# Optimization experiments

Hardware: AMD Instinct MI355X
Metric: run time of the kernel (lower is better)

Reference implementation:

```python
import jax, jax.numpy as jnp
import numpy as np

N, DM, F, G, FG = 4096, 512, 128, 8, 16
DH, DE, ES = 128, 256, 4
E = G * ES
GROUP_TOP_K, EXPERT_TOP_K = 2, 2
TEMP = 1.0
LN_EPS = 1e-5


def _ln(x, g, b):
    m = jnp.mean(x, axis=-1, keepdims=True)
    v = jnp.mean((x - m) ** 2, axis=-1, keepdims=True)
    return (x - m) * jax.lax.rsqrt(v + LN_EPS) * g + b


def _topk_softmax(logits, k):
    # faithful to torch _topk_softmax: softmax over top-k values, zeros elsewhere
    vals, idx = jax.lax.top_k(logits, k)
    w = jax.nn.softmax(vals, axis=-1)
    oh = jax.nn.one_hot(idx, logits.shape[-1], dtype=logits.dtype)  # [..., k, E]
    return jnp.einsum('...ke,...k->...e', oh, w)


def setup_inputs() -> dict:
    key = jax.random.key(0)
    ks = iter(jax.random.split(key, 32))
    n = lambda shape, s=0.02: jax.random.normal(next(ks), shape, dtype=jnp.float32) * s
    d = {
        'hidden': jax.random.normal(next(ks), (N, DM), dtype=jnp.float32),
        'feat': jax.random.normal(next(ks), (N, F), dtype=jnp.float32),
        # pre_ln
        'pre_ln_g': jnp.ones((DM,), jnp.float32), 'pre_ln_b': jnp.zeros((DM,), jnp.float32),
        # router_hidden_encoder: LN(DM) -> Lin(DM,DH) -> GELU -> Lin(DH,DH)
        'rh_ln_g': jnp.ones((DM,), jnp.float32), 'rh_ln_b': jnp.zeros((DM,), jnp.float32),
        'rh_w1': n((DM, DH)), 'rh_b1': jnp.zeros((DH,), jnp.float32),
        'rh_w2': n((DH, DH)), 'rh_b2': jnp.zeros((DH,), jnp.float32),
        # stage_feature_encoder: LN(F) -> Lin(F,DH) -> GELU -> Lin(DH,DH)
        'sf_ln_g': jnp.ones((F,), jnp.float32), 'sf_ln_b': jnp.zeros((F,), jnp.float32),
        'sf_w1': n((F, DH)), 'sf_b1': jnp.zeros((DH,), jnp.float32),
        'sf_w2': n((DH, DH)), 'sf_b2': jnp.zeros((DH,), jnp.float32),
        # group_feature_encoders (stacked over G): LN(FG) -> Lin(FG,DH) -> GELU -> Lin(DH,DH)
        'gf_ln_g': jnp.ones((G, FG), jnp.float32), 'gf_ln_b': jnp.zeros((G, FG), jnp.float32),
        'gf_w1': n((G, FG, DH)), 'gf_b1': jnp.zeros((G, DH), jnp.float32),
        'gf_w2': n((G, DH, DH)), 'gf_b2': jnp.zeros((G, DH), jnp.float32),
        # per_group_scorer (ScalarRouter): Lin(4DH,DH) -> GELU -> Lin(DH,1)
        'pgs_w1': n((4 * DH, DH)), 'pgs_b1': jnp.zeros((DH,), jnp.float32),
        'pgs_w2': n((DH,)), 'pgs_b2': jnp.zeros((), jnp.float32),
        # intra_routers (stacked over G): Lin(4DH,DH) -> GELU -> Lin(DH,ES)
        'ir_w1': n((G, 4 * DH, DH)), 'ir_b1': jnp.zeros((G, DH), jnp.float32),
        'ir_w2': n((G, DH, ES)), 'ir_b2': jnp.zeros((G, ES), jnp.float32),
        # experts (stacked over E = G*ES, group-major): Lin(DM,DE) -> GELU -> Lin(DE,DM)
        'ex_w1': n((E, DM, DE)), 'ex_b1': jnp.zeros((E, DE), jnp.float32),
        'ex_w2': n((E, DE, DM)), 'ex_b2': jnp.zeros((E, DM), jnp.float32),
    }
    return d


def reference(hidden, feat, pre_ln_g, pre_ln_b, rh_ln_g, rh_ln_b, rh_w1, rh_b1, rh_w2, rh_b2,
              sf_ln_g, sf_ln_b, sf_w1, sf_b1, sf_w2, sf_b2,
              gf_ln_g, gf_ln_b, gf_w1, gf_b1, gf_w2, gf_b2,
              pgs_w1, pgs_b1, pgs_w2, pgs_b2,
              ir_w1, ir_b1, ir_w2, ir_b2,
              ex_w1, ex_b1, ex_w2, ex_b2):
    # expert input (pre-LN hidden)
    h_norm = _ln(hidden, pre_ln_g, pre_ln_b)                         # [N, DM]

    # factorized router encoders
    h_enc = jax.nn.gelu(_ln(hidden, rh_ln_g, rh_ln_b) @ rh_w1 + rh_b1) @ rh_w2 + rh_b2   # [N, DH]
    s_enc = jax.nn.gelu(_ln(feat, sf_ln_g, sf_ln_b) @ sf_w1 + sf_b1) @ sf_w2 + sf_b2     # [N, DH]
    gfeat = feat.reshape(N, G, FG)                                    # disjoint contiguous group features
    g_h = jax.nn.gelu(jnp.einsum('ngf,gfh->ngh', _ln(gfeat, gf_ln_g, gf_ln_b), gf_w1) + gf_b1)
    g_enc = jnp.einsum('ngh,ghk->ngk', g_h, gf_w2) + gf_b2            # [N, G, DH]

    hB = jnp.broadcast_to(h_enc[:, None, :], (N, G, DH))
    sB = jnp.broadcast_to(s_enc[:, None, :], (N, G, DH))
    router_in = jnp.concatenate([hB, sB, g_enc, hB * g_enc], axis=-1)  # [N, G, 4DH]

    # per-group scalar scores -> group logits -> top-k scatter softmax
    pg_h = jax.nn.gelu(jnp.einsum('ngi,ih->ngh', router_in, pgs_w1) + pgs_b1)
    group_logits = (jnp.einsum('ngh,h->ng', pg_h, pgs_w2) + pgs_b2) / max(TEMP, 1e-6)    # [N, G]
    group_w = _topk_softmax(group_logits, GROUP_TOP_K)                 # [N, G]

    # intra-group expert routers -> top-k scatter softmax over expert_scale
    ir_h = jax.nn.gelu(jnp.einsum('ngi,gih->ngh', router_in, ir_w1) + ir_b1)
    intra_logits = jnp.einsum('ngh,ghe->nge', ir_h, ir_w2) + ir_b2     # [N, G, ES]
    intra_w = _topk_softmax(intra_logits, EXPERT_TOP_K)                # [N, G, ES]

    comb_w = (group_w[:, :, None] * intra_w).reshape(N, E)             # group-major expert order

    # per-expert GELU MLPs on pre-LN hidden (dense compute, sparse weights)
    eh = jax.nn.gelu(jnp.einsum('nd,edh->neh', h_norm, ex_w1) + ex_b1) # [N, E, DE]
    eo = jnp.einsum('neh,ehd->ned', eh, ex_w2) + ex_b2                 # [N, E, DM]
    out = jnp.einsum('ne,ned->nd', comb_w, eo)                         # [N, DM]
    return out
```

## Files before the change

kernel.cpp:

```cpp
#include <hip/hip_runtime.h>
#include <hip/hip_bf16.h>
#include <math.h>

#define N_TOK 4096
#define DM 512
#define FDIM 128
#define G 8
#define FG 16
#define DH 128
#define DE 256
#define ES 4
#define E_EXP 32
#define LN_EPS 1e-5f
#define BT 32

typedef __attribute__((ext_vector_type(8))) short bf16x8;
typedef __attribute__((ext_vector_type(4))) float f32x4;

#define MFMA16(a, b, c) __builtin_amdgcn_mfma_f32_16x16x32_bf16((a), (b), (c), 0, 0, 0)

__device__ __forceinline__ float gelu_t(float x) {
    const float c = 0.7978845608028654f;
    float x3 = x * x * x;
    return 0.5f * x * (1.0f + tanhf(c * (x + 0.044715f * x3)));
}

__device__ __forceinline__ short f2bf(float f) {
    __hip_bfloat16 h = __float2bfloat16(f);
    return *reinterpret_cast<short*>(&h);
}
__device__ __forceinline__ float bf2f(short s) {
    __hip_bfloat16 h = *reinterpret_cast<__hip_bfloat16*>(&s);
    return __bfloat162float(h);
}
__device__ __forceinline__ void split3(float x, short& h, short& m, short& l) {
    h = f2bf(x);
    float r = x - bf2f(h);
    m = f2bf(r);
    float r2 = r - bf2f(m);
    l = f2bf(r2);
}

__global__ void k_ln_hidden(const float* __restrict__ hidden,
                            const float* __restrict__ pg, const float* __restrict__ pb,
                            const float* __restrict__ rg, const float* __restrict__ rb,
                            __hip_bfloat16* __restrict__ h_normb, float* __restrict__ hL) {
    int n = blockIdx.x;
    int j = threadIdx.x;
    const float* x = hidden + (size_t)n * DM;
    float v0 = x[j], v1 = x[j + 256];
    float s = v0 + v1, q = v0 * v0 + v1 * v1;
#pragma unroll
    for (int o = 32; o; o >>= 1) { s += __shfl_down(s, o); q += __shfl_down(q, o); }
    __shared__ float red[8];
    int w = j >> 6;
    if ((j & 63) == 0) { red[w] = s; red[4 + w] = q; }
    __syncthreads();
    float sum = red[0] + red[1] + red[2] + red[3];
    float sq  = red[4] + red[5] + red[6] + red[7];
    float m = sum * (1.0f / DM);
    float var = sq * (1.0f / DM) - m * m;
    float rs = rsqrtf(var + LN_EPS);
    float t0 = (v0 - m) * rs, t1 = (v1 - m) * rs;
    size_t base = (size_t)n * DM;
    h_normb[base + j]       = __float2bfloat16(t0 * pg[j]       + pb[j]);
    h_normb[base + j + 256] = __float2bfloat16(t1 * pg[j + 256] + pb[j + 256]);
    hL[base + j]           = t0 * rg[j]       + rb[j];
    hL[base + j + 256]     = t1 * rg[j + 256] + rb[j + 256];
}

struct ConvJob { const float* src; short* dh; short* dm; short* dl;
                 int KB, NB, Kreal, plain, blk0; };
struct ConvJobs { ConvJob j[10]; };

__global__ void k_conv_all(ConvJobs J) {
    int b = blockIdx.x;
    int ji = 0;
#pragma unroll
    for (int i = 1; i < 10; i++) if (b >= J.j[i].blk0) ji = i;
    const ConvJob jb = J.j[ji];
    int rel = b - jb.blk0;
    int mat = rel / jb.KB, kb = rel % jb.KB;
    int ncols = jb.NB * 16;
    const float* s = jb.src + (size_t)mat * jb.Kreal * ncols;
    size_t dbase = ((size_t)mat * jb.KB + kb) * jb.NB * 512;
    for (int p = threadIdx.x; p < jb.NB * 64; p += 256) {
        int nb = p >> 6, lane = p & 63;
        int row0 = kb * 32 + ((lane >> 4) << 3);
        int col = nb * 16 + (lane & 15);
        if (jb.plain) {
            union { short sh[8]; uint4 v; } t;
#pragma unroll
            for (int j = 0; j < 8; j++) {
                float x = (row0 + j < jb.Kreal) ? s[(size_t)(row0 + j) * ncols + col] : 0.f;
                t.sh[j] = f2bf(x);
            }
            *(uint4*)&jb.dh[dbase + (size_t)p * 8] = t.v;
        } else {
            union { short sh[8]; uint4 v; } hi, mi, lo;
#pragma unroll
            for (int j = 0; j < 8; j++) {
                float x = (row0 + j < jb.Kreal) ? s[(size_t)(row0 + j) * ncols + col] : 0.f;
                split3(x, hi.sh[j], mi.sh[j], lo.sh[j]);
            }
            *(uint4*)&jb.dh[dbase + (size_t)p * 8] = hi.v;
            *(uint4*)&jb.dm[dbase + (size_t)p * 8] = mi.v;
            *(uint4*)&jb.dl[dbase + (size_t)p * 8] = lo.v;
        }
    }
}

template <int KB_TOT, bool DO_LN>
__device__ __forceinline__ void enc2_body(
        int bx, char* smem,
        const float* __restrict__ X,
        const float* __restrict__ lng, const float* __restrict__ lnb,
        const short* __restrict__ W1h, const short* __restrict__ W1m, const short* __restrict__ W1l,
        const float* __restrict__ B1,
        const short* __restrict__ W2h, const short* __restrict__ W2m, const short* __restrict__ W2l,
        const float* __restrict__ B2,
        float* __restrict__ Y) {
    constexpr int K = KB_TOT * 32;
    const int n0 = bx * 32;
    const int tid = threadIdx.x;
    const int wave = tid >> 6, lane = tid & 63;
    const int quad = lane >> 4, lm = lane & 15;
    const int mt = wave & 1;
    const int ngb = (wave >> 1) * 4;

    short (*Ah)[132] = (short(*)[132])smem;
    short (*Am)[132] = (short(*)[132])(smem + 32 * 132 * 2);
    short (*Al)[132] = (short(*)[132])(smem + 2 * 32 * 132 * 2);

    f32x4 acc[4];
#pragma unroll
    for (int i = 0; i < 4; i++) acc[i] = (f32x4)(0.f);

    if (DO_LN) {
        for (int idx = tid; idx < 1024; idx += 256) {
            int row = idx >> 5, c4 = (idx & 31) * 4;
            float4 v = *(const float4*)&X[(size_t)(n0 + row) * K + c4];
            float s = v.x + v.y + v.z + v.w;
            float q = v.x * v.x + v.y * v.y + v.z * v.z + v.w * v.w;
#pragma unroll
            for (int o = 16; o; o >>= 1) { s += __shfl_xor(s, o); q += __shfl_xor(q, o); }
            float mean = s * (1.0f / 128.0f);
            float var = q * (1.0f / 128.0f) - mean * mean;
            float rs = rsqrtf(var + LN_EPS);
            float xv[4] = {(v.x - mean) * rs * lng[c4 + 0] + lnb[c4 + 0],
                           (v.y - mean) * rs * lng[c4 + 1] + lnb[c4 + 1],
                           (v.z - mean) * rs * lng[c4 + 2] + lnb[c4 + 2],
                           (v.w - mean) * rs * lng[c4 + 3] + lnb[c4 + 3]};
#pragma unroll
            for (int j = 0; j < 4; j++) {
                short h, m, l; split3(xv[j], h, m, l);
                Ah[row][c4 + j] = h; Am[row][c4 + j] = m; Al[row][c4 + j] = l;
            }
        }
        __syncthreads();
#pragma unroll
        for (int kb = 0; kb < KB_TOT; kb++) {
            bf16x8 ah = *(const bf16x8*)&Ah[mt * 16 + lm][kb * 32 + quad * 8];
            bf16x8 am = *(const bf16x8*)&Am[mt * 16 + lm][kb * 32 + quad * 8];
            bf16x8 al = *(const bf16x8*)&Al[mt * 16 + lm][kb * 32 + quad * 8];
#pragma unroll
            for (int nt = 0; nt < 4; nt++) {
                size_t bi = (((size_t)kb * 8 + ngb + nt) * 64 + lane) * 8;
                bf16x8 bh = *(const bf16x8*)&W1h[bi];
                bf16x8 bm = *(const bf16x8*)&W1m[bi];
                bf16x8 bl = *(const bf16x8*)&W1l[bi];
                acc[nt] = MFMA16(al, bh, acc[nt]);
                acc[nt] = MFMA16(am, bm, acc[nt]);
                acc[nt] = MFMA16(ah, bl, acc[nt]);
                acc[nt] = MFMA16(am, bh, acc[nt]);
                acc[nt] = MFMA16(ah, bm, acc[nt]);
                acc[nt] = MFMA16(ah, bh, acc[nt]);
            }
        }
    } else {
        for (int kb = 0; kb < KB_TOT; kb++) {
            const float* xs = X + (size_t)(n0 + mt * 16 + lm) * K + kb * 32 + quad * 8;
            float4 x0 = *(const float4*)xs, x1 = *(const float4*)(xs + 4);
            float xv[8] = {x0.x, x0.y, x0.z, x0.w, x1.x, x1.y, x1.z, x1.w};
            bf16x8 ah, am, al;
#pragma unroll
            for (int j = 0; j < 8; j++) {
                short h, m, l; split3(xv[j], h, m, l);
                ah[j] = h; am[j] = m; al[j] = l;
            }
#pragma unroll
            for (int nt = 0; nt < 4; nt++) {
                size_t bi = (((size_t)kb * 8 + ngb + nt) * 64 + lane) * 8;
                bf16x8 bh = *(const bf16x8*)&W1h[bi];
                bf16x8 bm = *(const bf16x8*)&W1m[bi];
                bf16x8 bl = *(const bf16x8*)&W1l[bi];
                acc[nt] = MFMA16(al, bh, acc[nt]);
                acc[nt] = MFMA16(am, bm, acc[nt]);
                acc[nt] = MFMA16(ah, bl, acc[nt]);
                acc[nt] = MFMA16(am, bh, acc[nt]);
                acc[nt] = MFMA16(ah, bm, acc[nt]);
                acc[nt] = MFMA16(ah, bh, acc[nt]);
            }
        }
    }
    __syncthreads();
#pragma unroll
    for (int nt = 0; nt < 4; nt++) {
        int col = (ngb + nt) * 16 + lm;
        float b1 = B1[col];
#pragma unroll
        for (int r = 0; r < 4; r++) {
            int row = mt * 16 + quad * 4 + r;
            short h, m, l; split3(gelu_t(acc[nt][r] + b1), h, m, l);
            Ah[row][col] = h; Am[row][col] = m; Al[row][col] = l;
        }
    }
    __syncthreads();
    f32x4 acc2[4];
#pragma unroll
    for (int i = 0; i < 4; i++) acc2[i] = (f32x4)(0.f);
#pragma unroll
    for (int kb = 0; kb < 4; kb++) {
        bf16x8 ah = *(const bf16x8*)&Ah[mt * 16 + lm][kb * 32 + quad * 8];
        bf16x8 am = *(const bf16x8*)&Am[mt * 16 + lm][kb * 32 + quad * 8];
        bf16x8 al = *(const bf16x8*)&Al[mt * 16 + lm][kb * 32 + quad * 8];
#pragma unroll
        for (int nt = 0; nt < 4; nt++) {
            size_t bi = (((size_t)kb * 8 + ngb + nt) * 64 + lane) * 8;
            bf16x8 bh = *(const bf16x8*)&W2h[bi];
            bf16x8 bm = *(const bf16x8*)&W2m[bi];
            bf16x8 bl = *(const bf16x8*)&W2l[bi];
            acc2[nt] = MFMA16(al, bh, acc2[nt]);
            acc2[nt] = MFMA16(am, bm, acc2[nt]);
            acc2[nt] = MFMA16(ah, bl, acc2[nt]);
            acc2[nt] = MFMA16(am, bh, acc2[nt]);
            acc2[nt] = MFMA16(ah, bm, acc2[nt]);
            acc2[nt] = MFMA16(ah, bh, acc2[nt]);
        }
    }
#pragma unroll
    for (int nt = 0; nt < 4; nt++) {
        int col = (ngb + nt) * 16 + lm;
        float b2 = B2[col];
#pragma unroll
        for (int r = 0; r < 4; r++) {
            int row = mt * 16 + quad * 4 + r;
            Y[(size_t)(n0 + row) * DH + col] = acc2[nt][r] + b2;
        }
    }
}

__device__ __forceinline__ void genc_one(
        int bx, int g, char* smem,
        const float* __restrict__ feat,
        const float* __restrict__ gln_g, const float* __restrict__ gln_b,
        const short* __restrict__ W1h, const short* __restrict__ W1m, const short* __restrict__ W1l,
        const float* __restrict__ gb1,
        const short* __restrict__ W2h, const short* __restrict__ W2m, const short* __restrict__ W2l,
        const float* __restrict__ gb2,
        float* __restrict__ g_enc) {
    const int n0 = bx * 32;
    const int tid = threadIdx.x;
    const int wave = tid >> 6, lane = tid & 63;
    const int quad = lane >> 4, lm = lane & 15;
    const int mt = wave & 1;
    const int ngb = (wave >> 1) * 4;

    short (*Ah)[132] = (short(*)[132])smem;
    short (*Am)[132] = (short(*)[132])(smem + 8448);
    short (*Al)[132] = (short(*)[132])(smem + 2 * 8448);

    {
        int t = tid >> 3, sub = tid & 7;
        const float* fr = feat + (size_t)(n0 + t) * FDIM + g * FG;
        float xv[FG];
        float mean = 0.f;
#pragma unroll
        for (int i = 0; i < FG; i++) { xv[i] = fr[i]; mean += xv[i]; }
        mean *= (1.0f / FG);
        float var = 0.f;
#pragma unroll
        for (int i = 0; i < FG; i++) { float d = xv[i] - mean; var += d * d; }
        var *= (1.0f / FG);
        float rs = rsqrtf(var + LN_EPS);
#pragma unroll
        for (int j = 0; j < 2; j++) {
            int i = sub * 2 + j;
            float xn = (xv[i] - mean) * rs * gln_g[g * FG + i] + gln_b[g * FG + i];
            short h, m, l; split3(xn, h, m, l);
            Ah[t][i] = h; Am[t][i] = m; Al[t][i] = l;
            Ah[t][16 + i] = 0; Am[t][16 + i] = 0; Al[t][16 + i] = 0;
        }
    }
    __syncthreads();
    f32x4 acc[4];
#pragma unroll
    for (int i = 0; i < 4; i++) acc[i] = (f32x4)(0.f);
    {
        bf16x8 ah = *(const bf16x8*)&Ah[mt * 16 + lm][quad * 8];
        bf16x8 am = *(const bf16x8*)&Am[mt * 16 + lm][quad * 8];
        bf16x8 al = *(const bf16x8*)&Al[mt * 16 + lm][quad * 8];
#pragma unroll
        for (int nt = 0; nt < 4; nt++) {
            size_t bi = (((size_t)g * 8 + ngb + nt) * 64 + lane) * 8;
            bf16x8 bh = *(const bf16x8*)&W1h[bi];
            bf16x8 bm = *(const bf16x8*)&W1m[bi];
            bf16x8 bl = *(const bf16x8*)&W1l[bi];
            acc[nt] = MFMA16(al, bh, acc[nt]);
            acc[nt] = MFMA16(am, bm, acc[nt]);
            acc[nt] = MFMA16(ah, bl, acc[nt]);
            acc[nt] = MFMA16(am, bh, acc[nt]);
            acc[nt] = MFMA16(ah, bm, acc[nt]);
            acc[nt] = MFMA16(ah, bh, acc[nt]);
        }
    }
    __syncthreads();
#pragma unroll
    for (int nt = 0; nt < 4; nt++) {
        int col = (ngb + nt) * 16 + lm;
        float b1 = gb1[g * DH + col];
#pragma unroll
        for (int r = 0; r < 4; r++) {
            int row = mt * 16 + quad * 4 + r;
            short h, m, l; split3(gelu_t(acc[nt][r] + b1), h, m, l);
            Ah[row][col] = h; Am[row][col] = m; Al[row][col] = l;
        }
    }
    __syncthreads();
    f32x4 acc2[4];
#pragma unroll
    for (int i = 0; i < 4; i++) acc2[i] = (f32x4)(0.f);
#pragma unroll
    for (int kb = 0; kb < 4; kb++) {
        bf16x8 a2h = *(const bf16x8*)&Ah[mt * 16 + lm][kb * 32 + quad * 8];
        bf16x8 a2m = *(const bf16x8*)&Am[mt * 16 + lm][kb * 32 + quad * 8];
        bf16x8 a2l = *(const bf16x8*)&Al[mt * 16 + lm][kb * 32 + quad * 8];
#pragma unroll
        for (int nt = 0; nt < 4; nt++) {
            size_t bi = ((((size_t)g * 4 + kb) * 8 + ngb + nt) * 64 + lane) * 8;
            bf16x8 bh = *(const bf16x8*)&W2h[bi];
            bf16x8 bm = *(const bf16x8*)&W2m[bi];
            bf16x8 bl = *(const bf16x8*)&W2l[bi];
            acc2[nt] = MFMA16(a2l, bh, acc2[nt]);
            acc2[nt] = MFMA16(a2m, bm, acc2[nt]);
            acc2[nt] = MFMA16(a2h, bl, acc2[nt]);
            acc2[nt] = MFMA16(a2m, bh, acc2[nt]);
            acc2[nt] = MFMA16(a2h, bm, acc2[nt]);
            acc2[nt] = MFMA16(a2h, bh, acc2[nt]);
        }
    }
#pragma unroll
    for (int nt = 0; nt < 4; nt++) {
        int col = (ngb + nt) * 16 + lm;
        float b2 = gb2[g * DH + col];
#pragma unroll
        for (int r = 0; r < 4; r++) {
            int row = mt * 16 + quad * 4 + r;
            g_enc[((size_t)(n0 + row) * G + g) * DH + col] = acc2[nt][r] + b2;
        }
    }
}

__global__ __launch_bounds__(256) void k_enc_all(
        const float* __restrict__ hL, const float* __restrict__ feat,
        const float* __restrict__ sf_g, const float* __restrict__ sf_b,
        const float* __restrict__ gln_g, const float* __restrict__ gln_b,
        const short* Brh1H, const short* Brh1M, const short* Brh1L, const float* rh_b1,
        const short* Brh2H, const short* Brh2M, const short* Brh2L, const float* rh_b2,
        const short* Bsf1H, const short* Bsf1M, const short* Bsf1L, const float* sf_b1,
        const short* Bsf2H, const short* Bsf2M, const short* Bsf2L, const float* sf_b2,
        const short* Bgf1H, const short* Bgf1M, const short* Bgf1L, const float* gf_b1,
        const short* Bgf2H, const short* Bgf2M, const short* Bgf2L, const float* gf_b2,
        float* __restrict__ h_enc, float* __restrict__ s_enc, float* __restrict__ g_enc) {
    __shared__ __align__(16) char smem[3 * 8448];
    int bid = blockIdx.x;
    if (bid < 128)
        enc2_body<16, false>(bid, smem, hL, nullptr, nullptr,
                             Brh1H, Brh1M, Brh1L, rh_b1, Brh2H, Brh2M, Brh2L, rh_b2, h_enc);
    else if (bid < 256)
        enc2_body<4, true>(bid - 128, smem, feat, sf_g, sf_b,
                           Bsf1H, Bsf1M, Bsf1L, sf_b1, Bsf2H, Bsf2M, Bsf2L, sf_b2, s_enc);
    else {
        int idx = bid - 256;
        genc_one(idx >> 3, idx & 7, smem, feat, gln_g, gln_b,
                 Bgf1H, Bgf1M, Bgf1L, gf_b1, Bgf2H, Bgf2M, Bgf2L, gf_b2, g_enc);
    }
}

__global__ void k_stage_hs(const float* __restrict__ h_enc, const float* __restrict__ s_enc,
                           short* __restrict__ Ah, short* __restrict__ Am, short* __restrict__ Al) {
    int T16 = blockIdx.x;
    for (int slot = threadIdx.x; slot < 512; slot += 256) {
        int kb = slot >> 6, lane = slot & 63;
        int quad = lane >> 4, lm = lane & 15;
        int n = T16 * 16 + lm;
        int c0 = kb * 32 + quad * 8;
        const float* src = (c0 < 128) ? (h_enc + (size_t)n * DH + c0)
                                      : (s_enc + (size_t)n * DH + (c0 - 128));
        float4 x0 = *(const float4*)src;
        float4 x1 = *(const float4*)(src + 4);
        float xv[8] = {x0.x, x0.y, x0.z, x0.w, x1.x, x1.y, x1.z, x1.w};
        union { short sh[8]; uint4 v; } hi, mi, lo;
#pragma unroll
        for (int j = 0; j < 8; j++) split3(xv[j], hi.sh[j], mi.sh[j], lo.sh[j]);
        size_t base = ((size_t)T16 * 512 + slot) * 8;
        *(uint4*)&Ah[base] = hi.v;
        *(uint4*)&Am[base] = mi.v;
        *(uint4*)&Al[base] = lo.v;
    }
}

__global__ __launch_bounds__(256) void k_router_mfma(
        const short* __restrict__ AhsH, const short* __restrict__ AhsM, const short* __restrict__ AhsL,
        const float* __restrict__ h_enc, const float* __restrict__ g_enc,
        const short* __restrict__ BpgH, const short* __restrict__ BpgM, const short* __restrict__ BpgL,
        const short* __restrict__ BirH, const short* __restrict__ BirM, const short* __restrict__ BirL,
        const float* __restrict__ pb1, const float* __restrict__ pw2, const float* __restrict__ pb2,
        const float* __restrict__ ib1, const float* __restrict__ iw2, const float* __restrict__ ib2,
        float* __restrict__ glog, float* __restrict__ ilog) {
    const int g = blockIdx.x & 7;
    const int bx = blockIdx.x >> 3;
    const int tid = threadIdx.x;
    const int wave = tid >> 6, lane = tid & 63;
    const int quad = lane >> 4, lm = lane & 15;
    const bool is_pg = wave < 2;
    const int nbase = (wave & 1) * 4;
    const short* Bh = is_pg ? BpgH : (BirH + (size_t)g * 65536);
    const short* Bm = is_pg ? BpgM : (BirM + (size_t)g * 65536);
    const short* Bl = is_pg ? BpgL : (BirL + (size_t)g * 65536);
    const int n0 = bx * 32;

    __shared__ float ph[32][129];
    __shared__ float ih[32][129];

    f32x4 acc[2][4];
#pragma unroll
    for (int mt = 0; mt < 2; mt++)
#pragma unroll
        for (int nt = 0; nt < 4; nt++) acc[mt][nt] = (f32x4)(0.f);

    for (int kb = 0; kb < 16; kb++) {
        bf16x8 Ahf[2], Amf[2], Alf[2];
#pragma unroll
        for (int mt = 0; mt < 2; mt++) {
            if (kb < 8) {
                size_t ai = (((size_t)(2 * bx + mt) * 8 + kb) * 64 + lane) * 8;
                Ahf[mt] = *(const bf16x8*)&AhsH[ai];
                Amf[mt] = *(const bf16x8*)&AhsM[ai];
                Alf[mt] = *(const bf16x8*)&AhsL[ai];
            } else {
                int n = n0 + mt * 16 + lm;
                int c0 = (kb - 8) * 32 + quad * 8;
                float xv[8];
                if (c0 < 128) {
                    const float* gs = g_enc + ((size_t)n * G + g) * DH + c0;
                    float4 x0 = *(const float4*)gs, x1 = *(const float4*)(gs + 4);
                    xv[0]=x0.x; xv[1]=x0.y; xv[2]=x0.z; xv[3]=x0.w;
                    xv[4]=x1.x; xv[5]=x1.y; xv[6]=x1.z; xv[7]=x1.w;
                } else {
                    int c = c0 - 128;
                    const float* gs = g_enc + ((size_t)n * G + g) * DH + c;
                    const float* hsrc = h_enc + (size_t)n * DH + c;
                    float4 g0 = *(const float4*)gs, g1 = *(const float4*)(gs + 4);
                    float4 h0 = *(const float4*)hsrc, h1 = *(const float4*)(hsrc + 4);
                    xv[0]=h0.x*g0.x; xv[1]=h0.y*g0.y; xv[2]=h0.z*g0.z; xv[3]=h0.w*g0.w;
                    xv[4]=h1.x*g1.x; xv[5]=h1.y*g1.y; xv[6]=h1.z*g1.z; xv[7]=h1.w*g1.w;
                }
#pragma unroll
                for (int j = 0; j < 8; j++) {
                    short h, m, l; split3(xv[j], h, m, l);
                    Ahf[mt][j] = h; Amf[mt][j] = m; Alf[mt][j] = l;
                }
            }
        }
#pragma unroll
        for (int nt = 0; nt < 4; nt++) {
            int nb = nbase + nt;
            size_t bi = (((size_t)kb * 8 + nb) * 64 + lane) * 8;
            bf16x8 bh = *(const bf16x8*)&Bh[bi];
            bf16x8 bm = *(const bf16x8*)&Bm[bi];
            bf16x8 bl = *(const bf16x8*)&Bl[bi];
#pragma unroll
            for (int mt = 0; mt < 2; mt++) {
                acc[mt][nt] = MFMA16(Alf[mt], bh, acc[mt][nt]);
                acc[mt][nt] = MFMA16(Amf[mt], bm, acc[mt][nt]);
                acc[mt][nt] = MFMA16(Ahf[mt], bl, acc[mt][nt]);
                acc[mt][nt] = MFMA16(Amf[mt], bh, acc[mt][nt]);
                acc[mt][nt] = MFMA16(Ahf[mt], bm, acc[mt][nt]);
                acc[mt][nt] = MFMA16(Ahf[mt], bh, acc[mt][nt]);
            }
        }
    }

    float* dst = is_pg ? &ph[0][0] : &ih[0][0];
#pragma unroll
    for (int mt = 0; mt < 2; mt++)
#pragma unroll
    for (int nt = 0; nt < 4; nt++) {
        int col = (wave & 1) * 64 + nt * 16 + lm;
        float b1 = is_pg ? pb1[col] : ib1[g * DH + col];
#pragma unroll
        for (int r = 0; r < 4; r++) {
            int row = mt * 16 + quad * 4 + r;
            dst[row * 129 + col] = gelu_t(acc[mt][nt][r] + b1);
        }
    }
    __syncthreads();

    if (tid < 32) {
        float s = pb2[0];
        for (int i = 0; i < DH; i++) s += ph[tid][i] * pw2[i];
        glog[(size_t)(n0 + tid) * G + g] = s;
    } else if (tid >= 128) {
        int t = (tid - 128) >> 2, e = (tid - 128) & 3;
        float s = ib2[g * ES + e];
        const float* w = iw2 + (size_t)g * DH * ES;
        for (int i = 0; i < DH; i++) s += ih[t][i] * w[i * ES + e];
        ilog[((size_t)(n0 + t) * G + g) * ES + e] = s;
    }
}

__global__ void k_topk(const float* __restrict__ glog, const float* __restrict__ ilog,
                       int* __restrict__ cnt, int* __restrict__ toks, float* __restrict__ wgts) {
    int n = blockIdx.x * blockDim.x + threadIdx.x;
    if (n >= N_TOK) return;
    float gl[G];
#pragma unroll
    for (int g = 0; g < G; g++) gl[g] = glog[(size_t)n * G + g];
    int i1 = 0; float v1 = gl[0];
#pragma unroll
    for (int g = 1; g < G; g++) if (gl[g] > v1) { v1 = gl[g]; i1 = g; }
    int i2 = -1; float v2 = -1e30f;
#pragma unroll
    for (int g = 0; g < G; g++) if (g != i1 && gl[g] > v2) { v2 = gl[g]; i2 = g; }
    float eg = expf(v2 - v1);
    float den = 1.0f / (1.0f + eg);
    float gw_sel[2] = { den, eg * den };
    int g_sel[2] = { i1, i2 };
#pragma unroll
    for (int s = 0; s < 2; s++) {
        int g = g_sel[s]; float gw = gw_sel[s];
        float il[ES];
#pragma unroll
        for (int e = 0; e < ES; e++) il[e] = ilog[((size_t)n * G + g) * ES + e];
        int j1 = 0; float u1 = il[0];
#pragma unroll
        for (int e = 1; e < ES; e++) if (il[e] > u1) { u1 = il[e]; j1 = e; }
        int j2 = -1; float u2 = -1e30f;
#pragma unroll
        for (int e = 0; e < ES; e++) if (e != j1 && il[e] > u2) { u2 = il[e]; j2 = e; }
        float ei = expf(u2 - u1);
        float d2 = 1.0f / (1.0f + ei);
        int ex1 = g * ES + j1, ex2 = g * ES + j2;
        int p1 = atomicAdd(&cnt[ex1], 1);
        toks[(size_t)ex1 * N_TOK + p1] = n * 4 + s * 2;     wgts[(size_t)ex1 * N_TOK + p1] = gw * d2;
        int p2 = atomicAdd(&cnt[ex2], 1);
        toks[(size_t)ex2 * N_TOK + p2] = n * 4 + s * 2 + 1; wgts[(size_t)ex2 * N_TOK + p2] = gw * ei * d2;
    }
}

__global__ __launch_bounds__(512) void k_expert_mfma(
        const __hip_bfloat16* __restrict__ h_normb,
        const short* __restrict__ wB1, const float* __restrict__ eb1,
        const short* __restrict__ wB2, const float* __restrict__ eb2,
        const int* __restrict__ cnt, const int* __restrict__ toks,
        const float* __restrict__ wgts, float* __restrict__ part) {
    const int e = blockIdx.x & 31;
    const int slot = blockIdx.x >> 5;
    const int c = cnt[e];
    const int start = slot * BT;
    if (start >= c) return;
    const int m = min(BT, c - start);

    __shared__ short hs[BT][520];
    __shared__ short es[BT][264];
    __shared__ int   tok_s[BT];
    __shared__ float w_s[BT];

    const int tid = threadIdx.x;
    if (tid < BT) {
        bool ok = tid < m;
        tok_s[tid] = ok ? toks[(size_t)e * N_TOK + start + tid] : 0;
        w_s[tid]   = ok ? wgts[(size_t)e * N_TOK + start + tid] : 0.f;
    }
    __syncthreads();
    for (int idx = tid; idx < BT * 64; idx += 512) {
        int t = idx >> 6, ch = idx & 63;
        uint4 v = make_uint4(0, 0, 0, 0);
        if (t < m) v = *((const uint4*)(h_normb + (size_t)(tok_s[t] >> 2) * DM) + ch);
        *(uint4*)&hs[t][ch * 8] = v;
    }
    __syncthreads();

    const int wave = tid >> 6, lane = tid & 63;
    const int quad = lane >> 4, lm = lane & 15;

    {
        const int ng = wave * 2;
        f32x4 acc[2][2];
#pragma unroll
        for (int a = 0; a < 2; a++)
#pragma unroll
            for (int b = 0; b < 2; b++) acc[a][b] = (f32x4)(0.f);
        const short* w1e = wB1 + (size_t)e * DM * DE;
        for (int kb = 0; kb < 16; kb++) {
            bf16x8 a0 = *(const bf16x8*)&hs[lm][kb * 32 + quad * 8];
            bf16x8 a1 = *(const bf16x8*)&hs[16 + lm][kb * 32 + quad * 8];
            const short* wp = w1e + ((size_t)kb * 16 + ng) * 512 + lane * 8;
#pragma unroll
            for (int nt = 0; nt < 2; nt++) {
                bf16x8 b = *(const bf16x8*)(wp + nt * 512);
                acc[0][nt] = MFMA16(a0, b, acc[0][nt]);
                acc[1][nt] = MFMA16(a1, b, acc[1][nt]);
            }
        }
#pragma unroll
        for (int nt = 0; nt < 2; nt++) {
            int col = (ng + nt) * 16 + lm;
            float b1 = eb1[e * DE + col];
#pragma unroll
            for (int mt = 0; mt < 2; mt++)
#pragma unroll
            for (int r = 0; r < 4; r++) {
                int row = mt * 16 + quad * 4 + r;
                es[row][col] = f2bf(gelu_t(acc[mt][nt][r] + b1));
            }
        }
    }
    __syncthreads();

    {
        const int ng2 = wave * 4;
        f32x4 acc[2][4];
#pragma unroll
        for (int a = 0; a < 2; a++)
#pragma unroll
            for (int b = 0; b < 4; b++) acc[a][b] = (f32x4)(0.f);
        const short* w2e = wB2 + (size_t)e * DE * DM;
        for (int kb = 0; kb < 8; kb++) {
            bf16x8 a0 = *(const bf16x8*)&es[lm][kb * 32 + quad * 8];
            bf16x8 a1 = *(const bf16x8*)&es[16 + lm][kb * 32 + quad * 8];
            const short* wp = w2e + ((size_t)kb * 32 + ng2) * 512 + lane * 8;
#pragma unroll
            for (int nt = 0; nt < 4; nt++) {
                bf16x8 b = *(const bf16x8*)(wp + nt * 512);
                acc[0][nt] = MFMA16(a0, b, acc[0][nt]);
                acc[1][nt] = MFMA16(a1, b, acc[1][nt]);
            }
        }
        const float* b2 = eb2 + (size_t)e * DM;
#pragma unroll
        for (int mt = 0; mt < 2; mt++)
#pragma unroll
        for (int r = 0; r < 4; r++) {
            int row = mt * 16 + quad * 4 + r;
            if (row < m) {
                float w = w_s[row];
                float* prow = part + (size_t)tok_s[row] * DM;
#pragma unroll
                for (int nt = 0; nt < 4; nt++) {
                    int col = (ng2 + nt) * 16 + lm;
                    prow[col] = w * (acc[mt][nt][r] + b2[col]);
                }
            }
        }
    }
}

__global__ void k_reduce(const float* __restrict__ part, float* __restrict__ out) {
    int n = blockIdx.x;
    int j = threadIdx.x;
    const float4* p = (const float4*)(part + (size_t)n * 4 * DM);
    float4 a = p[j], b = p[128 + j], c = p[256 + j], d = p[384 + j];
    float4 r = make_float4(a.x + b.x + c.x + d.x, a.y + b.y + c.y + d.y,
                           a.z + b.z + c.z + d.z, a.w + b.w + c.w + d.w);
    ((float4*)(out + (size_t)n * DM))[j] = r;
}

extern "C" void kernel_launch(void* const* d_in, const int* in_sizes, int n_in,
                              void* d_out, int out_size, void* d_ws, size_t ws_size,
                              hipStream_t stream) {
    const float* hidden  = (const float*)d_in[0];
    const float* feat    = (const float*)d_in[1];
    const float* pre_g   = (const float*)d_in[2];
    const float* pre_b   = (const float*)d_in[3];
    const float* rh_g    = (const float*)d_in[4];
    const float* rh_b    = (const float*)d_in[5];
    const float* rh_w1   = (const float*)d_in[6];
    const float* rh_b1   = (const float*)d_in[7];
    const float* rh_w2   = (const float*)d_in[8];
    const float* rh_b2   = (const float*)d_in[9];
    const float* sf_g    = (const float*)d_in[10];
    const float* sf_b    = (const float*)d_in[11];
    const float* sf_w1   = (const float*)d_in[12];
    const float* sf_b1   = (const float*)d_in[13];
    const float* sf_w2   = (const float*)d_in[14];
    const float* sf_b2   = (const float*)d_in[15];
    const float* gln_g   = (const float*)d_in[16];
    const float* gln_b   = (const float*)d_in[17];
    const float* gf_w1   = (const float*)d_in[18];
    const float* gf_b1   = (const float*)d_in[19];
    const float* gf_w2   = (const float*)d_in[20];
    const float* gf_b2   = (const float*)d_in[21];
    const float* pgs_w1  = (const float*)d_in[22];
    const float* pgs_b1  = (const float*)d_in[23];
    const float* pgs_w2  = (const float*)d_in[24];
    const float* pgs_b2  = (const float*)d_in[25];
    const float* ir_w1   = (const float*)d_in[26];
    const float* ir_b1   = (const float*)d_in[27];
    const float* ir_w2   = (const float*)d_in[28];
    const float* ir_b2   = (const float*)d_in[29];
    const float* ex_w1   = (const float*)d_in[30];
    const float* ex_b1   = (const float*)d_in[31];
    const float* ex_w2   = (const float*)d_in[32];
    const float* ex_b2   = (const float*)d_in[33];
    float* out = (float*)d_out;

    char* w = (char*)d_ws;
    auto alloc = [&](size_t bytes) { void* r = (void*)w; w += (bytes + 255) & ~(size_t)255; return r; };
    __hip_bfloat16* h_normb = (__hip_bfloat16*)alloc((size_t)N_TOK * DM * 2);
    float* h_enc = (float*)alloc((size_t)N_TOK * DH * 4);
    float* s_enc = (float*)alloc((size_t)N_TOK * DH * 4);
    float* g_enc = (float*)alloc((size_t)N_TOK * G * DH * 4);
    float* glog  = (float*)alloc((size_t)N_TOK * G * 4);
    float* ilog  = (float*)alloc((size_t)N_TOK * G * ES * 4);
    float* wgts  = (float*)alloc((size_t)E_EXP * N_TOK * 4);
    short* wB1   = (short*)alloc((size_t)E_EXP * DM * DE * 2);
    short* wB2   = (short*)alloc((size_t)E_EXP * DE * DM * 2);
    short* AhsH  = (short*)alloc((size_t)N_TOK * 256 * 2);
    short* AhsM  = (short*)alloc((size_t)N_TOK * 256 * 2);
    short* AhsL  = (short*)alloc((size_t)N_TOK * 256 * 2);
    short* BpgH  = (short*)alloc((size_t)16 * 8 * 512 * 2);
    short* BpgM  = (short*)alloc((size_t)16 * 8 * 512 * 2);
    short* BpgL  = (short*)alloc((size_t)16 * 8 * 512 * 2);
    short* BirH  = (short*)alloc((size_t)G * 16 * 8 * 512 * 2);
    short* BirM  = (short*)alloc((size_t)G * 16 * 8 * 512 * 2);
    short* BirL  = (short*)alloc((size_t)G * 16 * 8 * 512 * 2);
    short* Brh1H = (short*)alloc((size_t)16 * 8 * 512 * 2);
    short* Brh1M = (short*)alloc((size_t)16 * 8 * 512 * 2);
    short* Brh1L = (short*)alloc((size_t)16 * 8 * 512 * 2);
    short* Brh2H = (short*)alloc((size_t)4 * 8 * 512 * 2);
    short* Brh2M = (short*)alloc((size_t)4 * 8 * 512 * 2);
    short* Brh2L = (short*)alloc((size_t)4 * 8 * 512 * 2);
    short* Bsf1H = (short*)alloc((size_t)4 * 8 * 512 * 2);
    short* Bsf1M = (short*)alloc((size_t)4 * 8 * 512 * 2);
    short* Bsf1L = (short*)alloc((size_t)4 * 8 * 512 * 2);
    short* Bsf2H = (short*)alloc((size_t)4 * 8 * 512 * 2);
    short* Bsf2M = (short*)alloc((size_t)4 * 8 * 512 * 2);
    short* Bsf2L = (short*)alloc((size_t)4 * 8 * 512 * 2);
    short* Bgf1H = (short*)alloc((size_t)G * 1 * 8 * 512 * 2);
    short* Bgf1M = (short*)alloc((size_t)G * 1 * 8 * 512 * 2);
    short* Bgf1L = (short*)alloc((size_t)G * 1 * 8 * 512 * 2);
    short* Bgf2H = (short*)alloc((size_t)G * 4 * 8 * 512 * 2);
    short* Bgf2M = (short*)alloc((size_t)G * 4 * 8 * 512 * 2);
    short* Bgf2L = (short*)alloc((size_t)G * 4 * 8 * 512 * 2);
    int* cnt     = (int*)alloc(E_EXP * 4);
    int* toks    = (int*)alloc((size_t)E_EXP * N_TOK * 4);
    char* uni   = (char*)alloc((size_t)N_TOK * 4 * DM * 4);
    float* hL   = (float*)uni;
    float* part = (float*)uni;

    hipMemsetAsync(cnt, 0, E_EXP * sizeof(int), stream);

    ConvJobs J;
    int b0 = 0;
    auto mkjob = [&](int i, const float* s, short* dh, short* dm, short* dl,
                     int KB, int NB, int Kreal, int plain, int nmat) {
        J.j[i] = ConvJob{s, dh, dm, dl, KB, NB, Kreal, plain, b0};
        b0 += KB * nmat;
    };
    mkjob(0, ex_w1, wB1, nullptr, nullptr, 16, 16, 512, 1, E_EXP);
    mkjob(1, ex_w2, wB2, nullptr, nullptr, 8, 32, 256, 1, E_EXP);
    mkjob(2, pgs_w1, BpgH, BpgM, BpgL, 16, 8, 512, 0, 1);
    mkjob(3, ir_w1, BirH, BirM, BirL, 16, 8, 512, 0, G);
    mkjob(4, rh_w1, Brh1H, Brh1M, Brh1L, 16, 8, 512, 0, 1);
    mkjob(5, rh_w2, Brh2H, Brh2M, Brh2L, 4, 8, 128, 0, 1);
    mkjob(6, sf_w1, Bsf1H, Bsf1M, Bsf1L, 4, 8, 128, 0, 1);
    mkjob(7, sf_w2, Bsf2H, Bsf2M, Bsf2L, 4, 8, 128, 0, 1);
    mkjob(8, gf_w1, Bgf1H, Bgf1M, Bgf1L, 1, 8, 16, 0, G);
    mkjob(9, gf_w2, Bgf2H, Bgf2M, Bgf2L, 4, 8, 128, 0, G);
    k_conv_all<<<b0, 256, 0, stream>>>(J);

    k_ln_hidden<<<N_TOK, 256, 0, stream>>>(hidden, pre_g, pre_b, rh_g, rh_b, h_normb, hL);

    k_enc_all<<<256 + (N_TOK / 32) * G, 256, 0, stream>>>(
        hL, feat, sf_g, sf_b, gln_g, gln_b,
        Brh1H, Brh1M, Brh1L, rh_b1, Brh2H, Brh2M, Brh2L, rh_b2,
        Bsf1H, Bsf1M, Bsf1L, sf_b1, Bsf2H, Bsf2M, Bsf2L, sf_b2,
        Bgf1H, Bgf1M, Bgf1L, gf_b1, Bgf2H, Bgf2M, Bgf2L, gf_b2,
        h_enc, s_enc, g_enc);

    k_stage_hs<<<N_TOK / 16, 256, 0, stream>>>(h_enc, s_enc, AhsH, AhsM, AhsL);

    k_router_mfma<<<(N_TOK / 32) * G, 256, 0, stream>>>(AhsH, AhsM, AhsL, h_enc, g_enc,
                                             BpgH, BpgM, BpgL, BirH, BirM, BirL,
                                             pgs_b1, pgs_w2, pgs_b2, ir_b1, ir_w2, ir_b2,
                                             glog, ilog);

    k_topk<<<N_TOK / 256, 256, 0, stream>>>(glog, ilog, cnt, toks, wgts);
    k_expert_mfma<<<(N_TOK / BT) * E_EXP, 512, 0, stream>>>(h_normb, wB1, ex_b1, wB2, ex_b2,
                                                            cnt, toks, wgts, part);
    k_reduce<<<N_TOK, 128, 0, stream>>>(part, out);
}
```

Measured before the change: 346.1 us.

## Stage router A-tiles in LDS with 64-token blocks and 8 waves

The router MFMA kernel now processes 64 tokens per block with 512 threads. The split bf16 A operands (including the on-the-fly g_enc and h*g products) are cooperatively staged into shared memory in chunks of four k-blocks, so each A fragment is loaded and split once per block instead of once per wave. This halves redundant B-weight traffic per token and removes duplicated split3 work. In exchange it adds barriers per chunk and a two-pass epilogue, and the 48KB of LDS may limit occupancy.

```diff
diff --git a/kernel.cpp b/kernel.cpp
--- a/kernel.cpp
+++ b/kernel.cpp
@@ -410,7 +410,7 @@
     }
 }
 
-__global__ __launch_bounds__(256) void k_router_mfma(
+__global__ __launch_bounds__(512) void k_router_mfma(
         const short* __restrict__ AhsH, const short* __restrict__ AhsM, const short* __restrict__ AhsL,
         const float* __restrict__ h_enc, const float* __restrict__ g_enc,
         const short* __restrict__ BpgH, const short* __restrict__ BpgM, const short* __restrict__ BpgL,
@@ -420,37 +420,40 @@
         float* __restrict__ glog, float* __restrict__ ilog) {
     const int g = blockIdx.x & 7;
     const int bx = blockIdx.x >> 3;
+    const int n0 = bx * 64;
     const int tid = threadIdx.x;
     const int wave = tid >> 6, lane = tid & 63;
     const int quad = lane >> 4, lm = lane & 15;
-    const bool is_pg = wave < 2;
-    const int nbase = (wave & 1) * 4;
+    const bool is_pg = wave < 4;
+    const int nbase = (wave & 3) * 2;
     const short* Bh = is_pg ? BpgH : (BirH + (size_t)g * 65536);
     const short* Bm = is_pg ? BpgM : (BirM + (size_t)g * 65536);
     const short* Bl = is_pg ? BpgL : (BirL + (size_t)g * 65536);
-    const int n0 = bx * 32;
-
-    __shared__ float ph[32][129];
-    __shared__ float ih[32][129];
-
-    f32x4 acc[2][4];
-#pragma unroll
-    for (int mt = 0; mt < 2; mt++)
-#pragma unroll
-        for (int nt = 0; nt < 4; nt++) acc[mt][nt] = (f32x4)(0.f);
-
-    for (int kb = 0; kb < 16; kb++) {
-        bf16x8 Ahf[2], Amf[2], Alf[2];
-#pragma unroll
-        for (int mt = 0; mt < 2; mt++) {
-            if (kb < 8) {
-                size_t ai = (((size_t)(2 * bx + mt) * 8 + kb) * 64 + lane) * 8;
-                Ahf[mt] = *(const bf16x8*)&AhsH[ai];
-                Amf[mt] = *(const bf16x8*)&AhsM[ai];
-                Alf[mt] = *(const bf16x8*)&AhsL[ai];
+
+    __shared__ __align__(16) char smem[49152];
+
+    f32x4 acc[4][2];
+#pragma unroll
+    for (int mt = 0; mt < 4; mt++)
+#pragma unroll
+        for (int nt = 0; nt < 2; nt++) acc[mt][nt] = (f32x4)(0.f);
+
+    for (int ch = 0; ch < 4; ch++) {
+        __syncthreads();
+        for (int idx = tid; idx < 1024; idx += 512) {
+            int kbl = idx >> 8, rem = idx & 255;
+            int t16 = rem >> 6, lane2 = rem & 63;
+            int gkb = ch * 4 + kbl;
+            size_t loff = (size_t)kbl * 4096 + t16 * 1024 + (size_t)lane2 * 16;
+            if (gkb < 8) {
+                int T16g = bx * 4 + t16;
+                size_t ai = (((size_t)T16g * 8 + gkb) * 64 + lane2) * 8;
+                *(uint4*)(smem + loff)         = *(const uint4*)&AhsH[ai];
+                *(uint4*)(smem + 16384 + loff) = *(const uint4*)&AhsM[ai];
+                *(uint4*)(smem + 32768 + loff) = *(const uint4*)&AhsL[ai];
             } else {
-                int n = n0 + mt * 16 + lm;
-                int c0 = (kb - 8) * 32 + quad * 8;
+                int n = n0 + t16 * 16 + (lane2 & 15);
+                int c0 = (gkb - 8) * 32 + (lane2 >> 4) * 8;
                 float xv[8];
                 if (c0 < 128) {
                     const float* gs = g_enc + ((size_t)n * G + g) * DH + c0;
@@ -466,57 +469,77 @@
                     xv[0]=h0.x*g0.x; xv[1]=h0.y*g0.y; xv[2]=h0.z*g0.z; xv[3]=h0.w*g0.w;
                     xv[4]=h1.x*g1.x; xv[5]=h1.y*g1.y; xv[6]=h1.z*g1.z; xv[7]=h1.w*g1.w;
                 }
-#pragma unroll
-                for (int j = 0; j < 8; j++) {
-                    short h, m, l; split3(xv[j], h, m, l);
-                    Ahf[mt][j] = h; Amf[mt][j] = m; Alf[mt][j] = l;
+                union { short sh[8]; uint4 v; } hi, mi, lo;
+#pragma unroll
+                for (int j = 0; j < 8; j++) split3(xv[j], hi.sh[j], mi.sh[j], lo.sh[j]);
+                *(uint4*)(smem + loff)         = hi.v;
+                *(uint4*)(smem + 16384 + loff) = mi.v;
+                *(uint4*)(smem + 32768 + loff) = lo.v;
+            }
+        }
+        __syncthreads();
+#pragma unroll
+        for (int kbl = 0; kbl < 4; kbl++) {
+            int kb = ch * 4 + kbl;
+            bf16x8 Ahf[4], Amf[4], Alf[4];
+#pragma unroll
+            for (int mt = 0; mt < 4; mt++) {
+                size_t loff = (size_t)kbl * 4096 + mt * 1024 + (size_t)lane * 16;
+                Ahf[mt] = *(const bf16x8*)(smem + loff);
+                Amf[mt] = *(const bf16x8*)(smem + 16384 + loff);
+                Alf[mt] = *(const bf16x8*)(smem + 32768 + loff);
+            }
+#pragma unroll
+            for (int nt = 0; nt < 2; nt++) {
+                int nb = nbase + nt;
+                size_t bi = (((size_t)kb * 8 + nb) * 64 + lane) * 8;
+                bf16x8 bh = *(const bf16x8*)&Bh[bi];
+                bf16x8 bm = *(const bf16x8*)&Bm[bi];
+                bf16x8 bl = *(const bf16x8*)&Bl[bi];
+#pragma unroll
+                for (int mt = 0; mt < 4; mt++) {
+                    acc[mt][nt] = MFMA16(Alf[mt], bh, acc[mt][nt]);
+                    acc[mt][nt] = MFMA16(Amf[mt], bm, acc[mt][nt]);
+                    acc[mt][nt] = MFMA16(Ahf[mt], bl, acc[mt][nt]);
+                    acc[mt][nt] = MFMA16(Amf[mt], bh, acc[mt][nt]);
+                    acc[mt][nt] = MFMA16(Ahf[mt], bm, acc[mt][nt]);
+                    acc[mt][nt] = MFMA16(Ahf[mt], bh, acc[mt][nt]);
                 }
             }
         }
-#pragma unroll
-        for (int nt = 0; nt < 4; nt++) {
-            int nb = nbase + nt;
-            size_t bi = (((size_t)kb * 8 + nb) * 64 + lane) * 8;
-            bf16x8 bh = *(const bf16x8*)&Bh[bi];
-            bf16x8 bm = *(const bf16x8*)&Bm[bi];
-            bf16x8 bl = *(const bf16x8*)&Bl[bi];
-#pragma unroll
-            for (int mt = 0; mt < 2; mt++) {
-                acc[mt][nt] = MFMA16(Alf[mt], bh, acc[mt][nt]);
-                acc[mt][nt] = MFMA16(Amf[mt], bm, acc[mt][nt]);
-                acc[mt][nt] = MFMA16(Ahf[mt], bl, acc[mt][nt]);
-                acc[mt][nt] = MFMA16(Amf[mt], bh, acc[mt][nt]);
-                acc[mt][nt] = MFMA16(Ahf[mt], bm, acc[mt][nt]);
-                acc[mt][nt] = MFMA16(Ahf[mt], bh, acc[mt][nt]);
-            }
-        }
-    }
-
-    float* dst = is_pg ? &ph[0][0] : &ih[0][0];
-#pragma unroll
-    for (int mt = 0; mt < 2; mt++)
-#pragma unroll
-    for (int nt = 0; nt < 4; nt++) {
-        int col = (wave & 1) * 64 + nt * 16 + lm;
-        float b1 = is_pg ? pb1[col] : ib1[g * DH + col];
-#pragma unroll
-        for (int r = 0; r < 4; r++) {
-            int row = mt * 16 + quad * 4 + r;
-            dst[row * 129 + col] = gelu_t(acc[mt][nt][r] + b1);
-        }
-    }
-    __syncthreads();
-
-    if (tid < 32) {
-        float s = pb2[0];
-        for (int i = 0; i < DH; i++) s += ph[tid][i] * pw2[i];
-        glog[(size_t)(n0 + tid) * G + g] = s;
-    } else if (tid >= 128) {
-        int t = (tid - 128) >> 2, e = (tid - 128) & 3;
-        float s = ib2[g * ES + e];
-        const float* w = iw2 + (size_t)g * DH * ES;
-        for (int i = 0; i < DH; i++) s += ih[t][i] * w[i * ES + e];
-        ilog[((size_t)(n0 + t) * G + g) * ES + e] = s;
+    }
+
+    float (*ph)[129] = (float(*)[129])smem;
+    float (*ih)[129] = (float(*)[129])(smem + 32 * 129 * 4);
+    for (int h = 0; h < 2; h++) {
+        __syncthreads();
+#pragma unroll
+        for (int mi = 0; mi < 2; mi++) {
+            int mt = 2 * h + mi;
+#pragma unroll
+            for (int nt = 0; nt < 2; nt++) {
+                int col = (nbase + nt) * 16 + lm;
+                float b1 = is_pg ? pb1[col] : ib1[g * DH + col];
+                float* dst = is_pg ? &ph[0][0] : &ih[0][0];
+#pragma unroll
+                for (int r = 0; r < 4; r++) {
+                    int row = mi * 16 + quad * 4 + r;
+                    dst[row * 129 + col] = gelu_t(acc[mt][nt][r] + b1);
+                }
+            }
+        }
+        __syncthreads();
+        if (tid < 32) {
+            float s = pb2[0];
+            for (int i = 0; i < DH; i++) s += ph[tid][i] * pw2[i];
+            glog[(size_t)(n0 + h * 32 + tid) * G + g] = s;
+        } else if (tid >= 128 && tid < 256) {
+            int t = (tid - 128) >> 2, e = (tid - 128) & 3;
+            float s = ib2[g * ES + e];
+            const float* w = iw2 + (size_t)g * DH * ES;
+            for (int i = 0; i < DH; i++) s += ih[t][i] * w[i * ES + e];
+            ilog[((size_t)(n0 + h * 32 + t) * G + g) * ES + e] = s;
+        }
     }
 }
 
@@ -792,7 +815,7 @@
 
     k_stage_hs<<<N_TOK / 16, 256, 0, stream>>>(h_enc, s_enc, AhsH, AhsM, AhsL);
 
-    k_router_mfma<<<(N_TOK / 32) * G, 256, 0, stream>>>(AhsH, AhsM, AhsL, h_enc, g_enc,
+    k_router_mfma<<<(N_TOK / 64) * G, 512, 0, stream>>>(AhsH, AhsM, AhsL, h_enc, g_enc,
                                              BpgH, BpgM, BpgL, BirH, BirM, BirL,
                                              pgs_b1, pgs_w2, pgs_b2, ir_b1, ir_w2, ir_b2,
                                              glog, ilog);
```

Result: faster. 335.8 us (-3.0%).
